# Performance work log

Measured on AMD Instinct MI355X. Metric: run time of the kernel, lower is better.

Reference implementation:

```python
import jax, jax.numpy as jnp
import numpy as np

B, N, F_IN, F_OUT = 8, 2048, 128, 128
NEG_BIG = -9e15
LEAKY_SLOPE = 0.01


def setup_inputs() -> dict:
    key = jax.random.key(0)
    k1, k2, k3, k4, k5 = jax.random.split(key, 5)
    features = jax.random.normal(k1, (B, N, F_IN), dtype=jnp.float32)
    adj_matrix = jax.random.randint(k2, (B, N, N), 0, 2, dtype=jnp.int32)
    mask = jnp.ones((B, N), dtype=jnp.float32)
    # linear: W [in,out], b [out]; attention: a [2*out] (no bias)
    W = jax.random.normal(k3, (F_IN, F_OUT), dtype=jnp.float32) / np.sqrt(F_IN)
    b = jnp.zeros((F_OUT,), dtype=jnp.float32)
    a = jax.random.normal(k4, (2 * F_OUT,), dtype=jnp.float32) / np.sqrt(2 * F_OUT)
    return {"features": features, "adj_matrix": adj_matrix, "mask": mask,
            "W": W, "b": b, "a": a}


def reference(features, adj_matrix, mask, W, b, a):
    h = jnp.einsum("bni,io->bno", features, W) + b  # [B,N,F_OUT]
    # attention(concat([h_i, h_j])) == h_i @ a_src + h_j @ a_dst
    a_src, a_dst = a[:F_OUT], a[F_OUT:]
    e = (h @ a_src)[:, :, None] + (h @ a_dst)[:, None, :]  # [B,N,N]
    e = jnp.where(e >= 0, e, LEAKY_SLOPE * e)  # leaky_relu
    scores = jnp.where(adj_matrix > 0, e, jnp.float32(NEG_BIG))
    attention = jax.nn.softmax(scores, axis=-1)
    aggregated = jnp.einsum("bnm,bmo->bno", attention, h)  # [B,N,F_OUT]
    aggregated = aggregated * mask[:, :, None]
    return aggregated
```

## Files before the change

### kernel.cpp

```cpp
#include <hip/hip_runtime.h>

#define BB 8
#define NN 2048
#define FF 128
#define RB 32
#define MT 128

typedef short bh8 __attribute__((ext_vector_type(8)));
typedef float fl4 __attribute__((ext_vector_type(4)));
typedef unsigned short u16;
typedef unsigned long long u64;

__device__ __forceinline__ u16 f2bf(float x) {
    unsigned u = __float_as_uint(x);
    return (u16)((u + 0x7FFFu + ((u >> 16) & 1u)) >> 16);
}

__global__ __launch_bounds__(256) void k_h(
    const float* __restrict__ feat, const float* __restrict__ W,
    const float* __restrict__ bias, const float* __restrict__ a,
    u16* __restrict__ htg, float* __restrict__ esrc, float* __restrict__ edst)
{
    __shared__ float fsh[8][FF];
    __shared__ float red[2][2][8];
    const int t = threadIdx.x;
    const long row0 = (long)blockIdx.x * 8;

    ((float4*)&fsh[0][0])[t] = ((const float4*)(feat + row0 * FF))[t];
    __syncthreads();

    const int o = t & 127;
    const int half = t >> 7;
    float acc[4] = {0.f, 0.f, 0.f, 0.f};
    #pragma unroll 4
    for (int k = 0; k < FF; ++k) {
        const float w = W[k * FF + o];
        #pragma unroll
        for (int r = 0; r < 4; ++r)
            acc[r] = fmaf(fsh[half * 4 + r][k], w, acc[r]);
    }
    const float bo = bias[o];
    const float as = a[o];
    const float ad = a[FF + o];
    float ps[4], pd[4];
    #pragma unroll
    for (int r = 0; r < 4; ++r) {
        acc[r] += bo;
        ps[r] = acc[r] * as;
        pd[r] = acc[r] * ad;
    }
    {
        const int bI = (int)(row0 >> 11);
        const int nloc = (int)(row0 & 2047) + half * 4;
        ushort4 hv;
        hv.x = f2bf(acc[0]); hv.y = f2bf(acc[1]);
        hv.z = f2bf(acc[2]); hv.w = f2bf(acc[3]);
        *(ushort4*)&htg[((long)bI * FF + o) * NN + nloc] = hv;
    }
    #pragma unroll
    for (int r = 0; r < 4; ++r) {
        #pragma unroll
        for (int off = 32; off > 0; off >>= 1) {
            ps[r] += __shfl_down(ps[r], off, 64);
            pd[r] += __shfl_down(pd[r], off, 64);
        }
    }
    const int wv = (t >> 6) & 1;
    if ((t & 63) == 0) {
        #pragma unroll
        for (int r = 0; r < 4; ++r) {
            red[half][wv][r]     = ps[r];
            red[half][wv][4 + r] = pd[r];
        }
    }
    __syncthreads();
    if (t < 16) {
        const int hh = t >> 3, idx = t & 7;
        const float v = red[hh][0][idx] + red[hh][1][idx];
        const long row = row0 + hh * 4 + (idx & 3);
        if (idx < 4) esrc[row] = v;
        else         edst[row] = v;
    }
}

__global__ __launch_bounds__(256) void k_pack(
    const int* __restrict__ adj, u64* __restrict__ bm)
{
    const int t = threadIdx.x;
    const int w = t >> 6, lane = t & 63;
    const long row0 = (long)blockIdx.x * 8;
    #pragma unroll 8
    for (int i = 0; i < 64; ++i) {
        const int row = 2 * w + (i >> 5);
        const int chunk = i & 31;
        const int av = adj[(row0 + row) * NN + chunk * 64 + lane];
        const u64 m64 = __ballot(av > 0);
        if (lane == 0) bm[(row0 + row) * 32 + chunk] = m64;
    }
}

__global__ __launch_bounds__(256, 2) void k_attn(
    const u64* __restrict__ bm, const float* __restrict__ mask,
    const u16* __restrict__ htg, const float* __restrict__ esrc,
    const float* __restrict__ edst, float* __restrict__ out)
{
    __shared__ float accbuf[4][RB][FF + 4];
    __shared__ float psum_sh[4][RB];

    const int t = threadIdx.x;
    const int b = blockIdx.x & 7;
    const int n0 = (blockIdx.x >> 3) * RB;
    const int w = t >> 6, lane = t & 63;
    const int lr = lane & 15, g = lane >> 4;

    float gmx = -3.4e38f;
    {
        const float4* edp = (const float4*)(edst + b * NN);
        #pragma unroll
        for (int i = 0; i < 8; ++i) {
            const float4 v = edp[lane + 64 * i];
            gmx = fmaxf(gmx, fmaxf(fmaxf(v.x, v.y), fmaxf(v.z, v.w)));
        }
        #pragma unroll
        for (int off = 32; off > 0; off >>= 1)
            gmx = fmaxf(gmx, __shfl_xor(gmx, off, 64));
    }

    const float es0 = esrc[b * NN + n0 + lr];
    const float es1 = esrc[b * NN + n0 + 16 + lr];
    const float tA = es0 + gmx; const float M0 = (tA >= 0.f) ? tA : 0.01f * tA;
    const float tB = es1 + gmx; const float M1 = (tB >= 0.f) ? tB : 0.01f * tB;

    const uint4* bmb = (const uint4*)(bm + ((long)b * NN + n0) * 32);
    const float* edb = edst + b * NN;
    const u16* hB = htg + (long)b * FF * NN;

    fl4 acc0[8], acc1[8];
    #pragma unroll
    for (int ct = 0; ct < 8; ++ct) {
        acc0[ct] = (fl4){0.f, 0.f, 0.f, 0.f};
        acc1[ct] = (fl4){0.f, 0.f, 0.f, 0.f};
    }
    float psum0 = 0.f, psum1 = 0.f;

    uint4 bmA0 = bmb[lr * 16 + w];
    uint4 bmA1 = bmb[(16 + lr) * 16 + w];

    #pragma unroll 1
    for (int it = 0; it < 4; ++it) {
        const int m0 = (w + 4 * it) * MT;
        const int base = m0 + g * 8;

        float4 ed[8];
        #pragma unroll
        for (int kc = 0; kc < 4; ++kc) {
            ed[2 * kc]     = *(const float4*)(edb + base + kc * 32);
            ed[2 * kc + 1] = *(const float4*)(edb + base + kc * 32 + 4);
        }
        bh8 bfA[8];
        #pragma unroll
        for (int ct = 0; ct < 8; ++ct)
            bfA[ct] = *(const bh8*)(hB + (long)(ct * 16 + lr) * NN + base);
        const int itn = (it + 1) & 3;
        uint4 bmB0 = bmb[lr * 16 + w + 4 * itn];
        uint4 bmB1 = bmb[(16 + lr) * 16 + w + 4 * itn];

        bh8 af0[4], af1[4];
        #pragma unroll
        for (int kc = 0; kc < 4; ++kc) {
            const unsigned w0 = (kc == 0) ? bmA0.x : (kc == 1) ? bmA0.y
                              : (kc == 2) ? bmA0.z : bmA0.w;
            const unsigned w1 = (kc == 0) ? bmA1.x : (kc == 1) ? bmA1.y
                              : (kc == 2) ? bmA1.z : bmA1.w;
            const unsigned by0 = (w0 >> (8 * g)) & 0xFFu;
            const unsigned by1 = (w1 >> (8 * g)) & 0xFFu;
            const float4 e0 = ed[2 * kc], e1 = ed[2 * kc + 1];
            const float ee[8] = {e0.x, e0.y, e0.z, e0.w, e1.x, e1.y, e1.z, e1.w};
            u16 p0[8], p1[8];
            #pragma unroll
            for (int j = 0; j < 8; ++j) {
                float x0 = es0 + ee[j]; x0 = (x0 >= 0.f) ? x0 : 0.01f * x0;
                float x1 = es1 + ee[j]; x1 = (x1 >= 0.f) ? x1 : 0.01f * x1;
                const float v0 = ((by0 >> j) & 1u) ? __expf(x0 - M0) : 0.f;
                const float v1 = ((by1 >> j) & 1u) ? __expf(x1 - M1) : 0.f;
                const u16 u0 = f2bf(v0), u1 = f2bf(v1);
                p0[j] = u0; p1[j] = u1;
                psum0 += __uint_as_float((unsigned)u0 << 16);
                psum1 += __uint_as_float((unsigned)u1 << 16);
            }
            af0[kc] = (bh8){(short)p0[0], (short)p0[1], (short)p0[2], (short)p0[3],
                            (short)p0[4], (short)p0[5], (short)p0[6], (short)p0[7]};
            af1[kc] = (bh8){(short)p1[0], (short)p1[1], (short)p1[2], (short)p1[3],
                            (short)p1[4], (short)p1[5], (short)p1[6], (short)p1[7]};
        }

        #pragma unroll
        for (int kc = 0; kc < 4; ++kc) {
            bh8 bfB[8];
            if (kc < 3) {
                #pragma unroll
                for (int ct = 0; ct < 8; ++ct)
                    bfB[ct] = *(const bh8*)(hB + (long)(ct * 16 + lr) * NN
                                            + base + (kc + 1) * 32);
            }
            #pragma unroll
            for (int ct = 0; ct < 8; ++ct) {
                acc0[ct] = __builtin_amdgcn_mfma_f32_16x16x32_bf16(af0[kc], bfA[ct], acc0[ct], 0, 0, 0);
                acc1[ct] = __builtin_amdgcn_mfma_f32_16x16x32_bf16(af1[kc], bfA[ct], acc1[ct], 0, 0, 0);
            }
            if (kc < 3) {
                #pragma unroll
                for (int ct = 0; ct < 8; ++ct) bfA[ct] = bfB[ct];
            }
        }
        bmA0 = bmB0; bmA1 = bmB1;
    }

    psum0 += __shfl_xor(psum0, 16, 64);
    psum0 += __shfl_xor(psum0, 32, 64);
    psum1 += __shfl_xor(psum1, 16, 64);
    psum1 += __shfl_xor(psum1, 32, 64);
    if (lane < 16) {
        psum_sh[w][lr] = psum0;
        psum_sh[w][16 + lr] = psum1;
    }

    #pragma unroll
    for (int ct = 0; ct < 8; ++ct)
        #pragma unroll
        for (int reg = 0; reg < 4; ++reg) {
            accbuf[w][g * 4 + reg][ct * 16 + lr]      = acc0[ct][reg];
            accbuf[w][16 + g * 4 + reg][ct * 16 + lr] = acc1[ct][reg];
        }
    __syncthreads();

    #pragma unroll
    for (int rep = 0; rep < 4; ++rep) {
        const int idx = t + 256 * rep;
        const int r = idx >> 5;
        const int c4 = (idx & 31) * 4;
        const float4 s0 = *(const float4*)&accbuf[0][r][c4];
        const float4 s1 = *(const float4*)&accbuf[1][r][c4];
        const float4 s2 = *(const float4*)&accbuf[2][r][c4];
        const float4 s3 = *(const float4*)&accbuf[3][r][c4];
        const float ps = psum_sh[0][r] + psum_sh[1][r] + psum_sh[2][r] + psum_sh[3][r];
        const float sc = mask[b * NN + n0 + r] / ps;
        float4 o;
        o.x = (s0.x + s1.x + s2.x + s3.x) * sc;
        o.y = (s0.y + s1.y + s2.y + s3.y) * sc;
        o.z = (s0.z + s1.z + s2.z + s3.z) * sc;
        o.w = (s0.w + s1.w + s2.w + s3.w) * sc;
        *(float4*)&out[((long)b * NN + n0 + r) * FF + c4] = o;
    }
}

extern "C" void kernel_launch(void* const* d_in, const int* in_sizes, int n_in,
                              void* d_out, int out_size, void* d_ws, size_t ws_size,
                              hipStream_t stream)
{
    const float* feat = (const float*)d_in[0];
    const int*   adj  = (const int*)d_in[1];
    const float* mask = (const float*)d_in[2];
    const float* W    = (const float*)d_in[3];
    const float* bias = (const float*)d_in[4];
    const float* a    = (const float*)d_in[5];
    float* out = (float*)d_out;

    u16*   htg  = (u16*)d_ws;
    float* esrc = (float*)(htg + (size_t)BB * FF * NN);
    float* edst = esrc + BB * NN;
    u64*   bmp  = (u64*)(edst + BB * NN);

    k_pack<<<BB * NN / 8, 256, 0, stream>>>(adj, bmp);
    k_h   <<<BB * NN / 8, 256, 0, stream>>>(feat, W, bias, a, htg, esrc, edst);
    k_attn<<<BB * (NN / RB), 256, 0, stream>>>(bmp, mask, htg, esrc, edst, out);
}
```

Before: 86.15 us.

## Factor exp of leaky-relu scores into precomputed per-column exps; repack adjacency per thread

The exp of the leaky-relu score is split into a product of per-row and per-column exponentials: exp(ed) and exp(0.01*ed) are precomputed once per column in k_h, and per-row constants plus a threshold select the branch. This removes the per-element transcendental from the attention inner loop and leaves a compare and a multiply. The adjacency packing kernel now has each thread read 64 contiguous ints with int4 loads and build its 64-bit mask, instead of a wave ballot per chunk. Bitmask prefetching across iterations is dropped and bf16 conversion uses paired intrinsics. The factored exponentials may overflow or underflow for large scores, which risks accuracy.

After: 92.04 us. +6.8%, slower.

```diff
diff --git a/kernel.cpp b/kernel.cpp
--- a/kernel.cpp
+++ b/kernel.cpp
@@ -1,4 +1,5 @@
 #include <hip/hip_runtime.h>
+#include <hip/hip_bf16.h>
 
 #define BB 8
 #define NN 2048
@@ -10,16 +11,40 @@
 typedef float fl4 __attribute__((ext_vector_type(4)));
 typedef unsigned short u16;
 typedef unsigned long long u64;
+typedef union { bh8 v; unsigned u[4]; } bh8u;
 
 __device__ __forceinline__ u16 f2bf(float x) {
     unsigned u = __float_as_uint(x);
     return (u16)((u + 0x7FFFu + ((u >> 16) & 1u)) >> 16);
 }
 
+__device__ __forceinline__ void loadB(bh8 (&buf)[8], const u16* hB, int lr, int kbase) {
+    #pragma unroll
+    for (int ct = 0; ct < 8; ++ct)
+        buf[ct] = *(const bh8*)(hB + (ct * 16 + lr) * NN + kbase);
+}
+
+__global__ __launch_bounds__(256) void k_pack(
+    const int* __restrict__ adj, u64* __restrict__ bm)
+{
+    const long gt = (long)blockIdx.x * 256 + threadIdx.x;
+    const int4* src = (const int4*)adj + gt * 16;
+    u64 m = 0;
+    #pragma unroll
+    for (int i = 0; i < 16; ++i) {
+        const int4 v = src[i];
+        const unsigned nib = (v.x > 0 ? 1u : 0u) | (v.y > 0 ? 2u : 0u)
+                           | (v.z > 0 ? 4u : 0u) | (v.w > 0 ? 8u : 0u);
+        m |= (u64)nib << (4 * i);
+    }
+    bm[gt] = m;
+}
+
 __global__ __launch_bounds__(256) void k_h(
     const float* __restrict__ feat, const float* __restrict__ W,
     const float* __restrict__ bias, const float* __restrict__ a,
-    u16* __restrict__ htg, float* __restrict__ esrc, float* __restrict__ edst)
+    u16* __restrict__ htg, float* __restrict__ esrc, float* __restrict__ edst,
+    float* __restrict__ eed, float* __restrict__ eed2)
 {
     __shared__ float fsh[8][FF];
     __shared__ float red[2][2][8];
@@ -78,31 +103,21 @@
         const int hh = t >> 3, idx = t & 7;
         const float v = red[hh][0][idx] + red[hh][1][idx];
         const long row = row0 + hh * 4 + (idx & 3);
-        if (idx < 4) esrc[row] = v;
-        else         edst[row] = v;
-    }
-}
-
-__global__ __launch_bounds__(256) void k_pack(
-    const int* __restrict__ adj, u64* __restrict__ bm)
-{
-    const int t = threadIdx.x;
-    const int w = t >> 6, lane = t & 63;
-    const long row0 = (long)blockIdx.x * 8;
-    #pragma unroll 8
-    for (int i = 0; i < 64; ++i) {
-        const int row = 2 * w + (i >> 5);
-        const int chunk = i & 31;
-        const int av = adj[(row0 + row) * NN + chunk * 64 + lane];
-        const u64 m64 = __ballot(av > 0);
-        if (lane == 0) bm[(row0 + row) * 32 + chunk] = m64;
+        if (idx < 4) {
+            esrc[row] = v;
+        } else {
+            edst[row] = v;
+            eed[row]  = __expf(v);
+            eed2[row] = __expf(0.01f * v);
+        }
     }
 }
 
 __global__ __launch_bounds__(256, 2) void k_attn(
     const u64* __restrict__ bm, const float* __restrict__ mask,
     const u16* __restrict__ htg, const float* __restrict__ esrc,
-    const float* __restrict__ edst, float* __restrict__ out)
+    const float* __restrict__ edst, const float* __restrict__ eed,
+    const float* __restrict__ eed2, float* __restrict__ out)
 {
     __shared__ float accbuf[4][RB][FF + 4];
     __shared__ float psum_sh[4][RB];
@@ -128,11 +143,14 @@
 
     const float es0 = esrc[b * NN + n0 + lr];
     const float es1 = esrc[b * NN + n0 + 16 + lr];
-    const float tA = es0 + gmx; const float M0 = (tA >= 0.f) ? tA : 0.01f * tA;
-    const float tB = es1 + gmx; const float M1 = (tB >= 0.f) ? tB : 0.01f * tB;
+    const float m0t = es0 + gmx; const float M0 = fmaxf(m0t, 0.01f * m0t);
+    const float m1t = es1 + gmx; const float M1 = fmaxf(m1t, 0.01f * m1t);
+    const float A0 = __expf(es0 - M0), Bv0 = __expf(0.01f * es0 - M0), T0 = __expf(-es0);
+    const float A1 = __expf(es1 - M1), Bv1 = __expf(0.01f * es1 - M1), T1 = __expf(-es1);
 
     const uint4* bmb = (const uint4*)(bm + ((long)b * NN + n0) * 32);
-    const float* edb = edst + b * NN;
+    const float* eeb  = eed  + b * NN;
+    const float* ee2b = eed2 + b * NN;
     const u16* hB = htg + (long)b * FF * NN;
 
     fl4 acc0[8], acc1[8];
@@ -143,66 +161,58 @@
     }
     float psum0 = 0.f, psum1 = 0.f;
 
-    uint4 bmA0 = bmb[lr * 16 + w];
-    uint4 bmA1 = bmb[(16 + lr) * 16 + w];
-
     #pragma unroll 1
     for (int it = 0; it < 4; ++it) {
-        const int m0 = (w + 4 * it) * MT;
-        const int base = m0 + g * 8;
-
-        float4 ed[8];
+        const int kb = (w + 4 * it) * MT + g * 8;
+        const uint4 bq0 = bmb[lr * 16 + (w + 4 * it)];
+        const uint4 bq1 = bmb[(16 + lr) * 16 + (w + 4 * it)];
+
+        bh8 bfA[8];
+        loadB(bfA, hB, lr, kb);
+
+        bh8 af0[4], af1[4];
         #pragma unroll
         for (int kc = 0; kc < 4; ++kc) {
-            ed[2 * kc]     = *(const float4*)(edb + base + kc * 32);
-            ed[2 * kc + 1] = *(const float4*)(edb + base + kc * 32 + 4);
-        }
-        bh8 bfA[8];
-        #pragma unroll
-        for (int ct = 0; ct < 8; ++ct)
-            bfA[ct] = *(const bh8*)(hB + (long)(ct * 16 + lr) * NN + base);
-        const int itn = (it + 1) & 3;
-        uint4 bmB0 = bmb[lr * 16 + w + 4 * itn];
-        uint4 bmB1 = bmb[(16 + lr) * 16 + w + 4 * itn];
-
-        bh8 af0[4], af1[4];
-        #pragma unroll
-        for (int kc = 0; kc < 4; ++kc) {
-            const unsigned w0 = (kc == 0) ? bmA0.x : (kc == 1) ? bmA0.y
-                              : (kc == 2) ? bmA0.z : bmA0.w;
-            const unsigned w1 = (kc == 0) ? bmA1.x : (kc == 1) ? bmA1.y
-                              : (kc == 2) ? bmA1.z : bmA1.w;
-            const unsigned by0 = (w0 >> (8 * g)) & 0xFFu;
-            const unsigned by1 = (w1 >> (8 * g)) & 0xFFu;
-            const float4 e0 = ed[2 * kc], e1 = ed[2 * kc + 1];
-            const float ee[8] = {e0.x, e0.y, e0.z, e0.w, e1.x, e1.y, e1.z, e1.w};
-            u16 p0[8], p1[8];
+            const unsigned q0 = (kc == 0) ? bq0.x : (kc == 1) ? bq0.y : (kc == 2) ? bq0.z : bq0.w;
+            const unsigned q1 = (kc == 0) ? bq1.x : (kc == 1) ? bq1.y : (kc == 2) ? bq1.z : bq1.w;
+            const unsigned by0 = (q0 >> (8 * g)) & 0xFFu;
+            const unsigned by1 = (q1 >> (8 * g)) & 0xFFu;
+            const float4 Ea = *(const float4*)(eeb + kb + kc * 32);
+            const float4 Eb = *(const float4*)(eeb + kb + kc * 32 + 4);
+            const float4 Fa = *(const float4*)(ee2b + kb + kc * 32);
+            const float4 Fb = *(const float4*)(ee2b + kb + kc * 32 + 4);
+            const float pe[8] = {Ea.x, Ea.y, Ea.z, Ea.w, Eb.x, Eb.y, Eb.z, Eb.w};
+            const float pf[8] = {Fa.x, Fa.y, Fa.z, Fa.w, Fb.x, Fb.y, Fb.z, Fb.w};
+            bh8u pa, pb;
+            float s0 = 0.f, s1 = 0.f;
             #pragma unroll
-            for (int j = 0; j < 8; ++j) {
-                float x0 = es0 + ee[j]; x0 = (x0 >= 0.f) ? x0 : 0.01f * x0;
-                float x1 = es1 + ee[j]; x1 = (x1 >= 0.f) ? x1 : 0.01f * x1;
-                const float v0 = ((by0 >> j) & 1u) ? __expf(x0 - M0) : 0.f;
-                const float v1 = ((by1 >> j) & 1u) ? __expf(x1 - M1) : 0.f;
-                const u16 u0 = f2bf(v0), u1 = f2bf(v1);
-                p0[j] = u0; p1[j] = u1;
-                psum0 += __uint_as_float((unsigned)u0 << 16);
-                psum1 += __uint_as_float((unsigned)u1 << 16);
+            for (int jj = 0; jj < 4; ++jj) {
+                const int j0 = 2 * jj, j1 = 2 * jj + 1;
+                const float v00 = ((by0 >> j0) & 1u) ? ((pe[j0] >= T0) ? A0 * pe[j0] : Bv0 * pf[j0]) : 0.f;
+                const float v01 = ((by0 >> j1) & 1u) ? ((pe[j1] >= T0) ? A0 * pe[j1] : Bv0 * pf[j1]) : 0.f;
+                const float v10 = ((by1 >> j0) & 1u) ? ((pe[j0] >= T1) ? A1 * pe[j0] : Bv1 * pf[j0]) : 0.f;
+                const float v11 = ((by1 >> j1) & 1u) ? ((pe[j1] >= T1) ? A1 * pe[j1] : Bv1 * pf[j1]) : 0.f;
+                float2 c0f; c0f.x = v00; c0f.y = v01;
+                float2 c1f; c1f.x = v10; c1f.y = v11;
+                __hip_bfloat162 r0 = __float22bfloat162_rn(c0f);
+                __hip_bfloat162 r1 = __float22bfloat162_rn(c1f);
+                const unsigned u0 = *reinterpret_cast<unsigned*>(&r0);
+                const unsigned u1 = *reinterpret_cast<unsigned*>(&r1);
+                pa.u[jj] = u0;
+                pb.u[jj] = u1;
+                s0 += __uint_as_float(u0 << 16) + __uint_as_float(u0 & 0xFFFF0000u);
+                s1 += __uint_as_float(u1 << 16) + __uint_as_float(u1 & 0xFFFF0000u);
             }
-            af0[kc] = (bh8){(short)p0[0], (short)p0[1], (short)p0[2], (short)p0[3],
-                            (short)p0[4], (short)p0[5], (short)p0[6], (short)p0[7]};
-            af1[kc] = (bh8){(short)p1[0], (short)p1[1], (short)p1[2], (short)p1[3],
-                            (short)p1[4], (short)p1[5], (short)p1[6], (short)p1[7]};
+            psum0 += s0;
+            psum1 += s1;
+            af0[kc] = pa.v;
+            af1[kc] = pb.v;
         }
 
         #pragma unroll
         for (int kc = 0; kc < 4; ++kc) {
             bh8 bfB[8];
-            if (kc < 3) {
-                #pragma unroll
-                for (int ct = 0; ct < 8; ++ct)
-                    bfB[ct] = *(const bh8*)(hB + (long)(ct * 16 + lr) * NN
-                                            + base + (kc + 1) * 32);
-            }
+            if (kc < 3) loadB(bfB, hB, lr, kb + (kc + 1) * 32);
             #pragma unroll
             for (int ct = 0; ct < 8; ++ct) {
                 acc0[ct] = __builtin_amdgcn_mfma_f32_16x16x32_bf16(af0[kc], bfA[ct], acc0[ct], 0, 0, 0);
@@ -213,7 +223,6 @@
                 for (int ct = 0; ct < 8; ++ct) bfA[ct] = bfB[ct];
             }
         }
-        bmA0 = bmB0; bmA1 = bmB1;
     }
 
     psum0 += __shfl_xor(psum0, 16, 64);
@@ -269,9 +278,11 @@
     u16*   htg  = (u16*)d_ws;
     float* esrc = (float*)(htg + (size_t)BB * FF * NN);
     float* edst = esrc + BB * NN;
-    u64*   bmp  = (u64*)(edst + BB * NN);
-
-    k_pack<<<BB * NN / 8, 256, 0, stream>>>(adj, bmp);
-    k_h   <<<BB * NN / 8, 256, 0, stream>>>(feat, W, bias, a, htg, esrc, edst);
-    k_attn<<<BB * (NN / RB), 256, 0, stream>>>(bmp, mask, htg, esrc, edst, out);
-}
+    float* eed  = edst + BB * NN;
+    float* eed2 = eed + BB * NN;
+    u64*   bmp  = (u64*)(eed2 + BB * NN);
+
+    k_pack<<<BB * NN * NN / 64 / 256, 256, 0, stream>>>(adj, bmp);
+    k_h   <<<BB * NN / 8, 256, 0, stream>>>(feat, W, bias, a, htg, esrc, edst, eed, eed2);
+    k_attn<<<BB * (NN / RB), 256, 0, stream>>>(bmp, mask, htg, esrc, edst, eed, eed2, out);
+}
```
